# Performance work log

Hardware: AMD Instinct MI355X
Metric: run time of the kernel (lower is better)

The kernel has to match this reference:

```python
import jax, jax.numpy as jnp
import numpy as np
import math

B, N, DIN, DH, DOUT = 32, 4096, 2, 512, 3
L = 3                      # num_hidden_modulation_matrices = num_layers - 2
LAT, MH, R = 512, 512, 5   # latent_dim, modulation_net_dim_hidden, UV_rank
W0, W0I = 30.0, 30.0
UV_END = 2 * DH * R * L
MOD_OUT = UV_END + DOUT * DH


def setup_inputs() -> dict:
    key = jax.random.key(0)
    ks = jax.random.split(key, 14)
    def unif(k, shape, s):
        return jax.random.uniform(k, shape, jnp.float32, -s, s)
    s0 = 1.0 / DIN                      # SIREN first-layer init bound
    sh = math.sqrt(6.0 / DH) / W0       # sqrt(c/dim_in)/w0 with c=6
    return {
        "x": jax.random.uniform(ks[0], (B, N, DIN), jnp.float32),
        "latent": jax.random.normal(ks[1], (B, LAT), jnp.float32),
        "W0": unif(ks[2], (DH, DIN), s0), "b0": unif(ks[3], (DH,), s0),
        "Wh": unif(ks[4], (L, DH, DH), sh), "bh": unif(ks[5], (L, DH), sh),
        "Wlast": unif(ks[6], (DOUT, DH), sh), "blast": unif(ks[7], (DOUT,), sh),
        "ln_g": jnp.ones((LAT,), jnp.float32), "ln_b": jnp.zeros((LAT,), jnp.float32),
        "Wm_in": jax.random.normal(ks[8], (MH, LAT), jnp.float32) * 0.02,
        "bm_in": jnp.zeros((MH,), jnp.float32),
        "Wr1": jax.random.normal(ks[9], (2, MH, MH), jnp.float32) * 0.02,
        "br1": jnp.zeros((2, MH), jnp.float32),
        "Wr2": jax.random.normal(ks[10], (2, MH, MH), jnp.float32) * 0.02,
        "br2": jnp.zeros((2, MH), jnp.float32),
        "Wm_out": jax.random.normal(ks[11], (MOD_OUT, MH), jnp.float32) * 0.02,
        "bm_out": jnp.zeros((MOD_OUT,), jnp.float32),
    }


def _modulation_net(latent, ln_g, ln_b, Wm_in, bm_in, Wr1, br1, Wr2, br2, Wm_out, bm_out):
    # LayerNorm(latent)
    mu = jnp.mean(latent, axis=-1, keepdims=True)
    var = jnp.var(latent, axis=-1, keepdims=True)
    h = (latent - mu) / jnp.sqrt(var + 1e-5) * ln_g + ln_b
    h = jax.nn.leaky_relu(h @ Wm_in.T + bm_in)
    for i in range(2):  # ResBlocks (use_batch_norm=False path)
        t = jax.nn.leaky_relu(h @ Wr1[i].T + br1[i])
        t = t @ Wr2[i].T + br2[i]
        h = jax.nn.leaky_relu(h + t)
    out = h @ Wm_out.T + bm_out                      # (B, MOD_OUT)
    UV = out[:, :UV_END].reshape(B, L, 2, DH, R)
    U, V = UV[:, :, 0], UV[:, :, 1]                  # (B, L, DH, R) each
    last_mod = jax.nn.sigmoid(out[:, UV_END:].reshape(B, DOUT, DH))
    return U, V, last_mod


def _forward(x, latent, W0_, b0, Wh, bh, Wlast, blast,
             ln_g, ln_b, Wm_in, bm_in, Wr1, br1, Wr2, br2, Wm_out, bm_out):
    U, V, last_mod = _modulation_net(latent, ln_g, ln_b, Wm_in, bm_in,
                                     Wr1, br1, Wr2, br2, Wm_out, bm_out)
    # first (unmodulated) SIREN layer
    h = jnp.sin(W0I * (x @ W0_.T + b0))              # (B, N, DH)
    # modulated hidden layers: per-sample low-rank weight scaling
    for i in range(L):
        G = jax.nn.sigmoid(jnp.einsum('bhr,bir->bhi', U[:, i], V[:, i]))  # (B, DH, DH)
        h = jnp.einsum('bni,bhi->bnh', h, (G + 1.0) * Wh[i]) + bh[i]
        h = jnp.sin(W0 * h)
    # modulated last layer (is_last: +0.5, no activation)
    out = jnp.einsum('bni,boi->bno', h, last_mod * Wlast) + blast + 0.5
    return out


def reference(x, latent, W0, b0, Wh, bh, Wlast, blast,
              ln_g, ln_b, Wm_in, bm_in, Wr1, br1, Wr2, br2, Wm_out, bm_out):
    return _forward(x, latent, W0, b0, Wh, bh, Wlast, blast,
                    ln_g, ln_b, Wm_in, bm_in, Wr1, br1, Wr2, br2, Wm_out, bm_out)
```

## Files before the change

kernel.cpp:

```cpp
#include <hip/hip_runtime.h>

#define UV_END_ 15360
#define MODOUT_ 16896

typedef __attribute__((ext_vector_type(8))) short s8v;
typedef __attribute__((ext_vector_type(4))) short s4v;
typedef __attribute__((ext_vector_type(8))) __bf16 bf16x8;
typedef __attribute__((ext_vector_type(4))) float f4v;

static __device__ __forceinline__ unsigned short f2bf(float f) {
  unsigned u = __float_as_uint(f);
  u += 0x7fffu + ((u >> 16) & 1u);
  return (unsigned short)(u >> 16);
}
static __device__ __forceinline__ float bf2f(unsigned short s) {
  return __uint_as_float(((unsigned)s) << 16);
}

static __device__ __forceinline__ float dot512i(const float* __restrict__ W,
                                                const float* __restrict__ hs) {
  const f4v* wr = (const f4v*)W;
  float a0 = 0, a1 = 0, a2 = 0, a3 = 0, a4 = 0, a5 = 0, a6 = 0, a7 = 0;
  #pragma unroll 4
  for (int c = 0; c < 128; c += 2) {
    f4v w0 = wr[c], w1 = wr[c + 1];
    a0 += w0.x * hs[c * 4 + 0]; a1 += w0.y * hs[c * 4 + 1];
    a2 += w0.z * hs[c * 4 + 2]; a3 += w0.w * hs[c * 4 + 3];
    a4 += w1.x * hs[c * 4 + 4]; a5 += w1.y * hs[c * 4 + 5];
    a6 += w1.z * hs[c * 4 + 6]; a7 += w1.w * hs[c * 4 + 7];
  }
  return ((a0 + a1) + (a2 + a3)) + ((a4 + a5) + (a6 + a7));
}

__global__ __launch_bounds__(512) void k_modnet(
    const float* __restrict__ latent, const float* __restrict__ ln_g,
    const float* __restrict__ ln_b,
    const float* __restrict__ Wm_in, const float* __restrict__ bm_in,
    const float* __restrict__ Wr1, const float* __restrict__ br1,
    const float* __restrict__ Wr2, const float* __restrict__ br2,
    float* __restrict__ hout) {
  __shared__ float A[512], B_[512], C[512];
  __shared__ float red[18];
  int b = blockIdx.x, t = threadIdx.x;
  int wv = t >> 6, ln = t & 63;
  float a0 = latent[b * 512 + t];
  float s = a0, q = a0 * a0;
  #pragma unroll
  for (int off = 32; off > 0; off >>= 1) {
    s += __shfl_down(s, off);
    q += __shfl_down(q, off);
  }
  if (ln == 0) { red[wv] = s; red[8 + wv] = q; }
  __syncthreads();
  if (t == 0) {
    float ss = 0, qq = 0;
    #pragma unroll
    for (int i = 0; i < 8; ++i) { ss += red[i]; qq += red[8 + i]; }
    float mean = ss * (1.0f / 512.0f);
    float var = qq * (1.0f / 512.0f) - mean * mean;
    red[16] = mean;
    red[17] = rsqrtf(var + 1e-5f);
  }
  __syncthreads();
  float mean = red[16], rstd = red[17];
  A[t] = (a0 - mean) * rstd * ln_g[t] + ln_b[t];
  __syncthreads();

  float acc = bm_in[t] + dot512i(Wm_in + (size_t)t * 512, A);
  B_[t] = acc > 0.f ? acc : 0.01f * acc;
  __syncthreads();
  acc = br1[t] + dot512i(Wr1 + (size_t)t * 512, B_);
  C[t] = acc > 0.f ? acc : 0.01f * acc;
  __syncthreads();
  acc = B_[t] + br2[t] + dot512i(Wr2 + (size_t)t * 512, C);
  A[t] = acc > 0.f ? acc : 0.01f * acc;
  __syncthreads();
  acc = br1[512 + t] + dot512i(Wr1 + 512 * 512 + (size_t)t * 512, A);
  C[t] = acc > 0.f ? acc : 0.01f * acc;
  __syncthreads();
  acc = A[t] + br2[512 + t] + dot512i(Wr2 + 512 * 512 + (size_t)t * 512, C);
  hout[b * 512 + t] = acc > 0.f ? acc : 0.01f * acc;
}

__global__ void k_modout(const float* __restrict__ h, const float* __restrict__ Wm,
                         const float* __restrict__ bm, const float* __restrict__ Wlast,
                         float* __restrict__ modout, float* __restrict__ Wfin) {
  int t = threadIdx.x;
  int o = blockIdx.x * 8 + (t >> 5);
  int b = t & 31;
  const f4v* wr = (const f4v*)(Wm + (size_t)o * 512);
  const f4v* hr = (const f4v*)(h + b * 512);
  float a0 = bm[o], a1 = 0, a2 = 0, a3 = 0;
  #pragma unroll 4
  for (int c = 0; c < 128; c += 2) {
    f4v w0 = wr[c], v0 = hr[c], w1 = wr[c + 1], v1 = hr[c + 1];
    a0 += w0.x * v0.x + w0.y * v0.y;
    a1 += w0.z * v0.z + w0.w * v0.w;
    a2 += w1.x * v1.x + w1.y * v1.y;
    a3 += w1.z * v1.z + w1.w * v1.w;
  }
  float acc = (a0 + a1) + (a2 + a3);
  if (o < UV_END_) {
    modout[(size_t)b * MODOUT_ + o] = acc;
  } else {
    int r = o - UV_END_;
    int od = r >> 9, hh = r & 511;
    float s = 1.f / (1.f + __expf(-acc));
    Wfin[(b * 3 + od) * 512 + hh] = s * Wlast[od * 512 + hh];
  }
}

__global__ void k_wprep(const float* __restrict__ modout, const float* __restrict__ Wh,
                        unsigned short* __restrict__ Wmod) {
  __shared__ float Vs[2560];
  __shared__ float Us[320];
  int ht = blockIdx.x, l = blockIdx.y, b = blockIdx.z, t = threadIdx.x;
  const float* mo = modout + (size_t)b * MODOUT_ + l * 5120;
  for (int i = t; i < 2560; i += 256) Vs[i] = mo[2560 + i];
  for (int i = t; i < 320; i += 256) Us[i] = mo[ht * 320 + i];
  __syncthreads();
  int w = t >> 6, lane = t & 63;
  int arow = lane & 15, kq = (lane >> 4) & 3;
  int hl = w * 16 + arow;
  int h = ht * 64 + hl;
  int g = ht * 4 + w;
  float u0 = Us[hl * 5], u1 = Us[hl * 5 + 1], u2 = Us[hl * 5 + 2],
        u3 = Us[hl * 5 + 3], u4 = Us[hl * 5 + 4];
  const float* whr = Wh + ((size_t)(l * 512 + h)) * 512;
  unsigned short* base = Wmod + (((size_t)(b * 3 + l)) << 18);
  for (int ks = 0; ks < 16; ++ks) {
    int i0 = ks * 32 + kq * 8;
    s8v pk;
    #pragma unroll
    for (int j = 0; j < 8; ++j) {
      int i = i0 + j;
      float gg = u0 * Vs[i * 5] + u1 * Vs[i * 5 + 1] + u2 * Vs[i * 5 + 2]
               + u3 * Vs[i * 5 + 3] + u4 * Vs[i * 5 + 4];
      float sg = 1.f / (1.f + __expf(-gg));
      float m = (sg + 1.f) * whr[i];
      pk[j] = (short)f2bf(m);
    }
    *(s8v*)(base + (((size_t)(g * 16 + ks)) << 9) + lane * 8) = pk;
  }
}

__global__ __launch_bounds__(512, 4) void k_main(
    const float* __restrict__ x, const float* __restrict__ W0w,
    const float* __restrict__ b0, const unsigned short* __restrict__ Wmod,
    const float* __restrict__ bh, const float* __restrict__ Wfin,
    const float* __restrict__ blast, float* __restrict__ outp) {
  __shared__ unsigned short hlds[64 * 512];
  const int bid = blockIdx.x;
  const int xcd = bid & 7, idx = bid >> 3;
  const int b = xcd * 4 + (idx >> 6);
  const int tile = idx & 63;
  const int t = threadIdx.x;
  const int lane = t & 63, wv = t >> 6;
  const int n0 = tile * 64;

  {
    int n = t >> 3;
    float x0 = x[((size_t)b * 4096 + n0 + n) * 2 + 0];
    float x1 = x[((size_t)b * 4096 + n0 + n) * 2 + 1];
    int swz = (n & 7) << 3;
    int cbase = (t & 7) * 64;
    for (int c = 0; c < 8; ++c) {
      int i0 = cbase + c * 8;
      s8v pk;
      #pragma unroll
      for (int j = 0; j < 8; ++j) {
        int i = i0 + j;
        float pre = x0 * W0w[i * 2] + x1 * W0w[i * 2 + 1] + b0[i];
        pk[j] = (short)f2bf(__sinf(30.0f * pre));
      }
      *(s8v*)&hlds[n * 512 + (i0 ^ swz)] = pk;
    }
  }
  __syncthreads();

  const int arow = lane & 15;
  const int kgrp = (lane >> 4) * 8;
  const int hbase = wv * 64;

  for (int l = 0; l < 3; ++l) {
    const unsigned short* wpf = Wmod + (((size_t)(b * 3 + l)) << 18)
                              + ((size_t)hbase << 9) + lane * 8;
    f4v acc[4][4];
    #pragma unroll
    for (int fi = 0; fi < 4; ++fi)
      #pragma unroll
      for (int fj = 0; fj < 4; ++fj) { f4v z = {0.f, 0.f, 0.f, 0.f}; acc[fi][fj] = z; }

    s8v abuf[2][4];
    #pragma unroll
    for (int fi = 0; fi < 4; ++fi)
      abuf[0][fi] = *(const s8v*)(wpf + fi * 8192);

    #pragma unroll
    for (int ks = 0; ks < 16; ++ks) {
      if (ks < 15) {
        #pragma unroll
        for (int fi = 0; fi < 4; ++fi)
          abuf[(ks + 1) & 1][fi] = *(const s8v*)(wpf + fi * 8192 + (ks + 1) * 512);
      }
      const int cur = ks & 1;
      int icol = ks * 32 + kgrp;
      bf16x8 bv[4];
      #pragma unroll
      for (int fj = 0; fj < 4; ++fj) {
        int n = fj * 16 + arow;
        bv[fj] = __builtin_bit_cast(bf16x8,
                   *(const s8v*)&hlds[n * 512 + (icol ^ ((n & 7) << 3))]);
      }
      __builtin_amdgcn_s_setprio(1);
      #pragma unroll
      for (int fi = 0; fi < 4; ++fi) {
        bf16x8 av = __builtin_bit_cast(bf16x8, abuf[cur][fi]);
        #pragma unroll
        for (int fj = 0; fj < 4; ++fj)
          acc[fi][fj] = __builtin_amdgcn_mfma_f32_16x16x32_bf16(av, bv[fj], acc[fi][fj], 0, 0, 0);
      }
      __builtin_amdgcn_s_setprio(0);
    }
    __syncthreads();

    const float* bhp = bh + l * 512;
    #pragma unroll
    for (int fi = 0; fi < 4; ++fi) {
      int hh = hbase + fi * 16 + (lane >> 4) * 4;
      float bv0 = bhp[hh], bv1 = bhp[hh + 1], bv2 = bhp[hh + 2], bv3 = bhp[hh + 3];
      #pragma unroll
      for (int fj = 0; fj < 4; ++fj) {
        int n = fj * 16 + arow;
        f4v a = acc[fi][fj];
        s4v pk;
        pk[0] = (short)f2bf(__sinf(30.f * (a.x + bv0)));
        pk[1] = (short)f2bf(__sinf(30.f * (a.y + bv1)));
        pk[2] = (short)f2bf(__sinf(30.f * (a.z + bv2)));
        pk[3] = (short)f2bf(__sinf(30.f * (a.w + bv3)));
        *(s4v*)&hlds[n * 512 + (hh ^ ((n & 7) << 3))] = pk;
      }
    }
    __syncthreads();
  }

  if (t < 192) {
    int n = t / 3, o = t - n * 3;
    const f4v* wf = (const f4v*)(Wfin + ((size_t)(b * 3 + o)) * 512);
    int swz = (n & 7) << 3;
    float acc = 0.f;
    #pragma unroll 4
    for (int c = 0; c < 64; ++c) {
      int i0 = c * 8;
      s8v hv = *(const s8v*)&hlds[n * 512 + (i0 ^ swz)];
      f4v w0 = wf[c * 2], w1 = wf[c * 2 + 1];
      acc += bf2f((unsigned short)hv[0]) * w0.x + bf2f((unsigned short)hv[1]) * w0.y
           + bf2f((unsigned short)hv[2]) * w0.z + bf2f((unsigned short)hv[3]) * w0.w
           + bf2f((unsigned short)hv[4]) * w1.x + bf2f((unsigned short)hv[5]) * w1.y
           + bf2f((unsigned short)hv[6]) * w1.z + bf2f((unsigned short)hv[7]) * w1.w;
    }
    outp[((size_t)b * 4096 + n0 + n) * 3 + o] = acc + blast[o] + 0.5f;
  }
}

extern "C" void kernel_launch(void* const* d_in, const int* in_sizes, int n_in,
                              void* d_out, int out_size, void* d_ws, size_t ws_size,
                              hipStream_t stream) {
  const float* x      = (const float*)d_in[0];
  const float* latent = (const float*)d_in[1];
  const float* W0w    = (const float*)d_in[2];
  const float* b0     = (const float*)d_in[3];
  const float* Wh     = (const float*)d_in[4];
  const float* bh     = (const float*)d_in[5];
  const float* Wlast  = (const float*)d_in[6];
  const float* blast  = (const float*)d_in[7];
  const float* ln_g   = (const float*)d_in[8];
  const float* ln_b   = (const float*)d_in[9];
  const float* Wm_in  = (const float*)d_in[10];
  const float* bm_in  = (const float*)d_in[11];
  const float* Wr1    = (const float*)d_in[12];
  const float* br1    = (const float*)d_in[13];
  const float* Wr2    = (const float*)d_in[14];
  const float* br2    = (const float*)d_in[15];
  const float* Wm_out = (const float*)d_in[16];
  const float* bm_out = (const float*)d_in[17];
  float* out = (float*)d_out;

  float* h1     = (float*)d_ws;
  float* modout = h1 + 32 * 512;
  float* Wfin   = modout + (size_t)32 * MODOUT_;
  unsigned short* Wmod = (unsigned short*)(Wfin + 32 * 3 * 512);

  k_modnet<<<32, 512, 0, stream>>>(latent, ln_g, ln_b, Wm_in, bm_in,
                                   Wr1, br1, Wr2, br2, h1);
  k_modout<<<2112, 256, 0, stream>>>(h1, Wm_out, bm_out, Wlast, modout, Wfin);
  k_wprep<<<dim3(8, 3, 32), 256, 0, stream>>>(modout, Wh, Wmod);
  k_main<<<2048, 512, 0, stream>>>(x, W0w, b0, Wmod, bh, Wfin, blast, out);
}
```

Before: 758.4 us.

## Coalesce modnet GEMVs via wave-per-row reductions and transpose hidden state

The modulation-net GEMVs now assign each wave 64 output rows and have its 64 lanes read one weight row contiguously, then reduce with cross-lane shuffles. Previously each thread walked its own 512-float row, giving strided, uncoalesced loads. The hidden state is written transposed so that k_modout reads coalesced across the batch lanes. The main kernel also drops its double-buffered A-fragment prefetch in favour of plain per-step loads, which lowers register pressure but may expose more load latency in the dominant MFMA loop.

```diff
diff --git a/kernel.cpp b/kernel.cpp
--- a/kernel.cpp
+++ b/kernel.cpp
@@ -17,19 +17,27 @@
   return __uint_as_float(((unsigned)s) << 16);
 }
 
-static __device__ __forceinline__ float dot512i(const float* __restrict__ W,
-                                                const float* __restrict__ hs) {
-  const f4v* wr = (const f4v*)W;
-  float a0 = 0, a1 = 0, a2 = 0, a3 = 0, a4 = 0, a5 = 0, a6 = 0, a7 = 0;
-  #pragma unroll 4
-  for (int c = 0; c < 128; c += 2) {
-    f4v w0 = wr[c], w1 = wr[c + 1];
-    a0 += w0.x * hs[c * 4 + 0]; a1 += w0.y * hs[c * 4 + 1];
-    a2 += w0.z * hs[c * 4 + 2]; a3 += w0.w * hs[c * 4 + 3];
-    a4 += w1.x * hs[c * 4 + 4]; a5 += w1.y * hs[c * 4 + 5];
-    a6 += w1.z * hs[c * 4 + 6]; a7 += w1.w * hs[c * 4 + 7];
-  }
-  return ((a0 + a1) + (a2 + a3)) + ((a4 + a5) + (a6 + a7));
+static __device__ __forceinline__ void gemv512(
+    const float* __restrict__ W, const float* __restrict__ bias,
+    const float* __restrict__ IN, const float* __restrict__ RES,
+    float* __restrict__ OUT, int wv, int ln) {
+  float iv0 = IN[ln * 8 + 0], iv1 = IN[ln * 8 + 1], iv2 = IN[ln * 8 + 2],
+        iv3 = IN[ln * 8 + 3], iv4 = IN[ln * 8 + 4], iv5 = IN[ln * 8 + 5],
+        iv6 = IN[ln * 8 + 6], iv7 = IN[ln * 8 + 7];
+  #pragma unroll 2
+  for (int oo = 0; oo < 64; ++oo) {
+    int o = wv * 64 + oo;
+    const f4v* wr = (const f4v*)(W + (size_t)o * 512 + ln * 8);
+    f4v w0 = wr[0], w1 = wr[1];
+    float p = w0.x * iv0 + w0.y * iv1 + w0.z * iv2 + w0.w * iv3
+            + w1.x * iv4 + w1.y * iv5 + w1.z * iv6 + w1.w * iv7;
+    #pragma unroll
+    for (int off = 1; off < 64; off <<= 1) p += __shfl_xor(p, off);
+    if (ln == 0) {
+      float acc = bias[o] + p + (RES ? RES[o] : 0.f);
+      OUT[o] = acc > 0.f ? acc : 0.01f * acc;
+    }
+  }
 }
 
 __global__ __launch_bounds__(512) void k_modnet(
@@ -38,7 +46,7 @@
     const float* __restrict__ Wm_in, const float* __restrict__ bm_in,
     const float* __restrict__ Wr1, const float* __restrict__ br1,
     const float* __restrict__ Wr2, const float* __restrict__ br2,
-    float* __restrict__ hout) {
+    float* __restrict__ houtT) {
   __shared__ float A[512], B_[512], C[512];
   __shared__ float red[18];
   int b = blockIdx.x, t = threadIdx.x;
@@ -66,38 +74,34 @@
   A[t] = (a0 - mean) * rstd * ln_g[t] + ln_b[t];
   __syncthreads();
 
-  float acc = bm_in[t] + dot512i(Wm_in + (size_t)t * 512, A);
-  B_[t] = acc > 0.f ? acc : 0.01f * acc;
-  __syncthreads();
-  acc = br1[t] + dot512i(Wr1 + (size_t)t * 512, B_);
-  C[t] = acc > 0.f ? acc : 0.01f * acc;
-  __syncthreads();
-  acc = B_[t] + br2[t] + dot512i(Wr2 + (size_t)t * 512, C);
-  A[t] = acc > 0.f ? acc : 0.01f * acc;
-  __syncthreads();
-  acc = br1[512 + t] + dot512i(Wr1 + 512 * 512 + (size_t)t * 512, A);
-  C[t] = acc > 0.f ? acc : 0.01f * acc;
-  __syncthreads();
-  acc = A[t] + br2[512 + t] + dot512i(Wr2 + 512 * 512 + (size_t)t * 512, C);
-  hout[b * 512 + t] = acc > 0.f ? acc : 0.01f * acc;
-}
-
-__global__ void k_modout(const float* __restrict__ h, const float* __restrict__ Wm,
+  gemv512(Wm_in, bm_in, A, nullptr, B_, wv, ln);
+  __syncthreads();
+  gemv512(Wr1, br1, B_, nullptr, C, wv, ln);
+  __syncthreads();
+  gemv512(Wr2, br2, C, B_, A, wv, ln);
+  __syncthreads();
+  gemv512(Wr1 + 512 * 512, br1 + 512, A, nullptr, C, wv, ln);
+  __syncthreads();
+  gemv512(Wr2 + 512 * 512, br2 + 512, C, A, B_, wv, ln);
+  __syncthreads();
+  houtT[t * 32 + b] = B_[t];
+}
+
+__global__ void k_modout(const float* __restrict__ hT, const float* __restrict__ Wm,
                          const float* __restrict__ bm, const float* __restrict__ Wlast,
                          float* __restrict__ modout, float* __restrict__ Wfin) {
   int t = threadIdx.x;
   int o = blockIdx.x * 8 + (t >> 5);
   int b = t & 31;
   const f4v* wr = (const f4v*)(Wm + (size_t)o * 512);
-  const f4v* hr = (const f4v*)(h + b * 512);
   float a0 = bm[o], a1 = 0, a2 = 0, a3 = 0;
   #pragma unroll 4
-  for (int c = 0; c < 128; c += 2) {
-    f4v w0 = wr[c], v0 = hr[c], w1 = wr[c + 1], v1 = hr[c + 1];
-    a0 += w0.x * v0.x + w0.y * v0.y;
-    a1 += w0.z * v0.z + w0.w * v0.w;
-    a2 += w1.x * v1.x + w1.y * v1.y;
-    a3 += w1.z * v1.z + w1.w * v1.w;
+  for (int c = 0; c < 128; ++c) {
+    f4v w = wr[c];
+    a0 += w.x * hT[(c * 4 + 0) * 32 + b];
+    a1 += w.y * hT[(c * 4 + 1) * 32 + b];
+    a2 += w.z * hT[(c * 4 + 2) * 32 + b];
+    a3 += w.w * hT[(c * 4 + 3) * 32 + b];
   }
   float acc = (a0 + a1) + (a2 + a3);
   if (o < UV_END_) {
@@ -191,19 +195,12 @@
       #pragma unroll
       for (int fj = 0; fj < 4; ++fj) { f4v z = {0.f, 0.f, 0.f, 0.f}; acc[fi][fj] = z; }
 
-    s8v abuf[2][4];
-    #pragma unroll
-    for (int fi = 0; fi < 4; ++fi)
-      abuf[0][fi] = *(const s8v*)(wpf + fi * 8192);
-
     #pragma unroll
     for (int ks = 0; ks < 16; ++ks) {
-      if (ks < 15) {
-        #pragma unroll
-        for (int fi = 0; fi < 4; ++fi)
-          abuf[(ks + 1) & 1][fi] = *(const s8v*)(wpf + fi * 8192 + (ks + 1) * 512);
-      }
-      const int cur = ks & 1;
+      s8v ab[4];
+      #pragma unroll
+      for (int fi = 0; fi < 4; ++fi)
+        ab[fi] = *(const s8v*)(wpf + fi * 8192 + ks * 512);
       int icol = ks * 32 + kgrp;
       bf16x8 bv[4];
       #pragma unroll
@@ -215,7 +212,7 @@
       __builtin_amdgcn_s_setprio(1);
       #pragma unroll
       for (int fi = 0; fi < 4; ++fi) {
-        bf16x8 av = __builtin_bit_cast(bf16x8, abuf[cur][fi]);
+        bf16x8 av = __builtin_bit_cast(bf16x8, ab[fi]);
         #pragma unroll
         for (int fj = 0; fj < 4; ++fj)
           acc[fi][fj] = __builtin_amdgcn_mfma_f32_16x16x32_bf16(av, bv[fj], acc[fi][fj], 0, 0, 0);
@@ -286,14 +283,14 @@
   const float* bm_out = (const float*)d_in[17];
   float* out = (float*)d_out;
 
-  float* h1     = (float*)d_ws;
-  float* modout = h1 + 32 * 512;
+  float* hT     = (float*)d_ws;
+  float* modout = hT + 32 * 512;
   float* Wfin   = modout + (size_t)32 * MODOUT_;
   unsigned short* Wmod = (unsigned short*)(Wfin + 32 * 3 * 512);
 
   k_modnet<<<32, 512, 0, stream>>>(latent, ln_g, ln_b, Wm_in, bm_in,
-                                   Wr1, br1, Wr2, br2, h1);
-  k_modout<<<2112, 256, 0, stream>>>(h1, Wm_out, bm_out, Wlast, modout, Wfin);
+                                   Wr1, br1, Wr2, br2, hT);
+  k_modout<<<2112, 256, 0, stream>>>(hT, Wm_out, bm_out, Wlast, modout, Wfin);
   k_wprep<<<dim3(8, 3, 32), 256, 0, stream>>>(modout, Wh, Wmod);
   k_main<<<2048, 512, 0, stream>>>(x, W0w, b0, Wmod, bh, Wfin, blast, out);
 }
```

New measurement: 753.6 us. Within noise of the previous version (-0.6%).
